# Performance work log

Hardware: AMD Instinct MI355X
Metric: run time of the kernel (lower is better)

The kernel has to match this reference:

```python
import jax, jax.numpy as jnp
import numpy as np

N_NODES = 50000
N_EDGES = 800000
FEAT = 64
HID = 128
N_TYPES = 4
N_REL = 3
N_LAYERS = 2
LN_EPS = 1e-5


def setup_inputs() -> dict:
    key = jax.random.key(0)
    ks = jax.random.split(key, 20)
    inp = {
        "z": jax.random.randint(ks[0], (N_NODES,), 0, 100, dtype=jnp.int32),
        "node_type": jax.random.randint(ks[1], (N_NODES,), 0, N_TYPES, dtype=jnp.int32),
        "edge_index": jax.random.randint(ks[2], (2, N_EDGES), 0, N_NODES, dtype=jnp.int32),
        "edge_type": jax.random.randint(ks[3], (N_EDGES,), 0, N_REL, dtype=jnp.int32),
        # learned parameters
        "z_embed": jax.random.normal(ks[4], (100, FEAT), jnp.float32),
        "enc_w1": jax.random.normal(ks[5], (N_TYPES, FEAT, HID), jnp.float32) * 0.05,
        "enc_b1": jnp.zeros((N_TYPES, HID), jnp.float32),
        "enc_w2": jax.random.normal(ks[6], (N_TYPES, HID, HID), jnp.float32) * 0.05,
        "enc_b2": jnp.zeros((N_TYPES, HID), jnp.float32),
        "lin_w": jax.random.normal(ks[7], (N_LAYERS, HID, HID), jnp.float32) * 0.05,
        "lin_b": jnp.zeros((N_LAYERS, HID), jnp.float32),
        "rel_w": jax.random.normal(ks[8], (N_LAYERS, N_REL, HID, HID), jnp.float32) * 0.05,
        "ln_g": jnp.ones((N_LAYERS, HID), jnp.float32),
        "ln_b": jnp.zeros((N_LAYERS, HID), jnp.float32),
        "reg_w": jax.random.normal(ks[9], (HID, 1), jnp.float32) * 0.05,
        "reg_b": jnp.zeros((1,), jnp.float32),
    }
    return inp


def _layer_norm(x, g, b):
    mu = jnp.mean(x, axis=-1, keepdims=True)
    var = jnp.mean((x - mu) ** 2, axis=-1, keepdims=True)
    return (x - mu) * jax.lax.rsqrt(var + LN_EPS) * g + b


def reference(z, node_type, edge_index, edge_type, z_embed, enc_w1, enc_b1,
              enc_w2, enc_b2, lin_w, lin_b, rel_w, ln_g, ln_b, reg_w, reg_b):
    n = z.shape[0]
    # FeatureBuilder (site_ads=None path): atomic-number embedding lookup
    raw = z_embed[z]  # [N, FEAT]
    # TypeSpecificEncoder: run all 4 type MLPs, select per node by node_type
    h = jax.nn.relu(jnp.einsum('nd,tdh->nth', raw, enc_w1) + enc_b1)  # [N,T,H]
    enc_all = jnp.einsum('nth,tho->nto', h, enc_w2) + enc_b2           # [N,T,H]
    x = jnp.take_along_axis(enc_all, node_type[:, None, None].astype(jnp.int32), axis=1)[:, 0, :]

    src, dst = edge_index[0], edge_index[1]
    deg = jax.ops.segment_sum(jnp.ones((edge_type.shape[0],), x.dtype), dst, num_segments=n)
    deg = jnp.clip(deg, 1.0, None)[:, None]  # [N,1]

    for l in range(N_LAYERS):
        out = jnp.zeros_like(x)
        x_src = x[src]  # [E, H] gathered source features
        for r in range(N_REL):
            mask = (edge_type == r).astype(x.dtype)[:, None]
            msg = (x_src * mask) @ rel_w[l, r]  # [E, H]
            out = out + jax.ops.segment_sum(msg, dst, num_segments=n)
        out = out / deg
        x = _layer_norm(x @ lin_w[l] + lin_b[l] + out, ln_g[l], ln_b[l])

    pooled = jnp.mean(x, axis=0)  # mean pooling, mask = all ones
    return pooled @ reg_w + reg_b  # [1]
```

## Files before the change

### kernel.cpp

```cpp
#include <hip/hip_runtime.h>

#define N_NODES 50000
#define N_EDGES 800000
#define FEAT 64
#define HID 128
#define N_TYPES 4
#define N_REL 3
#define N_LAYERS 2
#define LN_EPS 1e-5f
#define NROWS 50016
#define NG32 1563
#define CAP 64
#define NBKT 196
#define CAP1 4608
#define EPB 4096
#define BINCAP 56
#define NCOMBO 400
#define WT_STRIDE 136

typedef __attribute__((ext_vector_type(8))) short bf16x8;
typedef __attribute__((ext_vector_type(16))) float f32x16;

static __device__ inline unsigned short f2bf(float f) {
    unsigned int u = __float_as_uint(f);
    return (unsigned short)((u + 0x7fffu + ((u >> 16) & 1u)) >> 16);
}
static __device__ inline unsigned int packbf2(float lo, float hi) {
    return (unsigned int)f2bf(lo) | ((unsigned int)f2bf(hi) << 16);
}

__global__ __launch_bounds__(256) void combo_kernel(const int* __restrict__ z,
                                                    const int* __restrict__ nt,
                                                    unsigned short* __restrict__ combo) {
    int i = blockIdx.x * 256 + threadIdx.x;
    if (i < N_NODES) combo[i] = (unsigned short)(z[i] * 4 + nt[i]);
}

__global__ __launch_bounds__(256) void bin1_kernel(const int* __restrict__ src,
                                                   const int* __restrict__ dst,
                                                   const int* __restrict__ et,
                                                   int* __restrict__ bcnt,
                                                   int* __restrict__ bucket) {
    __shared__ int lbin[NBKT * BINCAP];
    __shared__ int lcnt[NBKT];
    __shared__ int lbase[NBKT];
    for (int i = threadIdx.x; i < NBKT; i += 256) lcnt[i] = 0;
    __syncthreads();
    int base = blockIdx.x * EPB;
#pragma unroll
    for (int i = 0; i < EPB / 256; ++i) {
        int e = base + i * 256 + threadIdx.x;
        if (e < N_EDGES) {
            int d = dst[e];
            int b = d >> 8;
            int v = src[e] | (et[e] << 16) | ((d & 255) << 18);
            int pos = atomicAdd(&lcnt[b], 1);
            if (pos < BINCAP) lbin[b * BINCAP + pos] = v;
        }
    }
    __syncthreads();
    if (threadIdx.x < NBKT) {
        int c = min(lcnt[threadIdx.x], BINCAP);
        lcnt[threadIdx.x] = c;
        lbase[threadIdx.x] = atomicAdd(&bcnt[threadIdx.x], c);
    }
    __syncthreads();
    int wv = threadIdx.x >> 6, ln = threadIdx.x & 63;
    for (int b = wv; b < NBKT; b += 4) {
        int c = lcnt[b];
        if (ln < c) {
            int gp = lbase[b] + ln;
            if (gp < CAP1) bucket[b * CAP1 + gp] = lbin[b * BINCAP + ln];
        }
    }
}

__global__ __launch_bounds__(256) void build2_kernel(const int* __restrict__ bcnt,
                                                     const int* __restrict__ bucket,
                                                     const unsigned short* __restrict__ combo,
                                                     int* __restrict__ cnt,
                                                     int* __restrict__ payload) {
    __shared__ int lcnt[256];
    lcnt[threadIdx.x] = 0;
    __syncthreads();
    int b = blockIdx.x;
    int n0 = b << 8;
    int cb = min(bcnt[b], CAP1);
    const int* bk = bucket + b * CAP1;
    for (int i = threadIdx.x; i < cb; i += 256) {
        int v = bk[i];
        int dl = (v >> 18) & 255;
        int sc = v & 0xffff;
        int pos = atomicAdd(&lcnt[dl], 1);
        if (pos < CAP)
            payload[((n0 + dl) << 6) + pos] = (v & 0x3FFFF) | ((int)combo[sc] << 18);
    }
    __syncthreads();
    int node = n0 + threadIdx.x;
    if (node < N_NODES) cnt[node] = min(lcnt[threadIdx.x], CAP);
}

__global__ __launch_bounds__(128) void enc_table_kernel(const float* __restrict__ z_embed,
                                                        const float* __restrict__ w1,
                                                        const float* __restrict__ b1,
                                                        const float* __restrict__ w2,
                                                        const float* __restrict__ b2,
                                                        unsigned short* __restrict__ xt) {
    int zi = blockIdx.x >> 2;
    int t = blockIdx.x & 3;
    int j = threadIdx.x;
    __shared__ float h[HID];
    float acc = b1[t * HID + j];
#pragma unroll 8
    for (int k = 0; k < FEAT; ++k)
        acc = fmaf(z_embed[zi * FEAT + k], w1[((size_t)t * FEAT + k) * HID + j], acc);
    h[j] = fmaxf(acc, 0.0f);
    __syncthreads();
    float acc2 = b2[t * HID + j];
#pragma unroll 8
    for (int k = 0; k < HID; ++k)
        acc2 = fmaf(h[k], w2[(size_t)t * HID * HID + k * HID + j], acc2);
    xt[blockIdx.x * HID + j] = f2bf(acc2);
}

__global__ __launch_bounds__(128) void rel_table_kernel(const unsigned short* __restrict__ xt,
                                                        const float* __restrict__ rel_w,
                                                        const float* __restrict__ lin_w,
                                                        const float* __restrict__ lin_b,
                                                        unsigned short* __restrict__ ytab,
                                                        float* __restrict__ lintab) {
    int c = blockIdx.x;
    int j = threadIdx.x;
    __shared__ float xrow[HID];
    xrow[j] = __uint_as_float((unsigned int)xt[c * HID + j] << 16);
    __syncthreads();
#pragma unroll 1
    for (int r = 0; r < N_REL; ++r) {
        float acc = 0.f;
        const float* W = rel_w + (size_t)r * HID * HID;
#pragma unroll 8
        for (int k = 0; k < HID; ++k) acc = fmaf(xrow[k], W[k * HID + j], acc);
        ytab[(size_t)(r * NCOMBO + c) * HID + j] = f2bf(acc);
    }
    float acc = lin_b[j];
#pragma unroll 8
    for (int k = 0; k < HID; ++k) acc = fmaf(xrow[k], lin_w[k * HID + j], acc);
    lintab[c * HID + j] = acc;
}

__global__ __launch_bounds__(256) void prep_weights_kernel(const float* __restrict__ rel_w,
                                                           const float* __restrict__ lin_w,
                                                           unsigned short* __restrict__ wbuf) {
    int idx = blockIdx.x * 256 + threadIdx.x;
    if (idx >= 2 * 4 * HID * HID) return;
    int k = idx & 127;
    int col = (idx >> 7) & 127;
    int lm = idx >> 14;
    int l = lm >> 2, mat = lm & 3;
    float w = (mat < 3) ? rel_w[(((size_t)l * 3 + mat) * HID + k) * HID + col]
                        : lin_w[((size_t)l * HID + k) * HID + col];
    wbuf[(size_t)lm * HID * WT_STRIDE + col * WT_STRIDE + k] = f2bf(w);
}

__global__ __launch_bounds__(256) void gather_ln1_kernel(
    const int* __restrict__ cnt, const int* __restrict__ payload,
    const uint4* __restrict__ ytab4, const float* __restrict__ lintab,
    const unsigned short* __restrict__ combo, const float* __restrict__ lng,
    const float* __restrict__ lnb, uint4* __restrict__ xb4) {
    int tid = blockIdx.x * 256 + threadIdx.x;
    int node = tid >> 4;
    int l16 = tid & 15;
    int cn = cnt[node];
    float inv = 1.0f / (float)max(cn, 1);
    const int* pl = payload + (node << 6);
    float a[8] = {};
    int e = 0;
    for (; e + 2 <= cn; e += 2) {
        int pA = pl[e], pB = pl[e + 1];
        uint4 vA = ytab4[((((pA >> 16) & 3) * NCOMBO + (pA >> 18)) << 4) + l16];
        uint4 vB = ytab4[((((pB >> 16) & 3) * NCOMBO + (pB >> 18)) << 4) + l16];
        a[0] += __uint_as_float(vA.x << 16) + __uint_as_float(vB.x << 16);
        a[1] += __uint_as_float(vA.x & 0xffff0000u) + __uint_as_float(vB.x & 0xffff0000u);
        a[2] += __uint_as_float(vA.y << 16) + __uint_as_float(vB.y << 16);
        a[3] += __uint_as_float(vA.y & 0xffff0000u) + __uint_as_float(vB.y & 0xffff0000u);
        a[4] += __uint_as_float(vA.z << 16) + __uint_as_float(vB.z << 16);
        a[5] += __uint_as_float(vA.z & 0xffff0000u) + __uint_as_float(vB.z & 0xffff0000u);
        a[6] += __uint_as_float(vA.w << 16) + __uint_as_float(vB.w << 16);
        a[7] += __uint_as_float(vA.w & 0xffff0000u) + __uint_as_float(vB.w & 0xffff0000u);
    }
    if (e < cn) {
        int p = pl[e];
        uint4 v = ytab4[((((p >> 16) & 3) * NCOMBO + (p >> 18)) << 4) + l16];
        a[0] += __uint_as_float(v.x << 16);
        a[1] += __uint_as_float(v.x & 0xffff0000u);
        a[2] += __uint_as_float(v.y << 16);
        a[3] += __uint_as_float(v.y & 0xffff0000u);
        a[4] += __uint_as_float(v.z << 16);
        a[5] += __uint_as_float(v.z & 0xffff0000u);
        a[6] += __uint_as_float(v.w << 16);
        a[7] += __uint_as_float(v.w & 0xffff0000u);
    }
    const float* lrow = lintab + (int)combo[node] * HID + l16 * 8;
    float v[8], s = 0.f, q = 0.f;
#pragma unroll
    for (int j = 0; j < 8; ++j) {
        v[j] = fmaf(a[j], inv, lrow[j]);
        s += v[j];
        q += v[j] * v[j];
    }
#pragma unroll
    for (int mk = 1; mk < 16; mk <<= 1) {
        s += __shfl_xor(s, mk);
        q += __shfl_xor(q, mk);
    }
    float mu = s * (1.0f / HID);
    float rstd = rsqrtf(q * (1.0f / HID) - mu * mu + LN_EPS);
    const float* g8 = lng + l16 * 8;
    const float* b8 = lnb + l16 * 8;
    uint4 w;
    w.x = packbf2((v[0] - mu) * rstd * g8[0] + b8[0], (v[1] - mu) * rstd * g8[1] + b8[1]);
    w.y = packbf2((v[2] - mu) * rstd * g8[2] + b8[2], (v[3] - mu) * rstd * g8[3] + b8[3]);
    w.z = packbf2((v[4] - mu) * rstd * g8[4] + b8[4], (v[5] - mu) * rstd * g8[5] + b8[5]);
    w.w = packbf2((v[6] - mu) * rstd * g8[6] + b8[6], (v[7] - mu) * rstd * g8[7] + b8[7]);
    xb4[(node << 4) + l16] = w;
}

__global__ __launch_bounds__(256) void gather3_kernel(const int* __restrict__ cnt,
                                                      const int* __restrict__ payload,
                                                      const uint4* __restrict__ xb4,
                                                      uint4* __restrict__ s0,
                                                      uint4* __restrict__ s1,
                                                      uint4* __restrict__ s2) {
    int tid = blockIdx.x * 256 + threadIdx.x;
    int node = tid >> 4;
    int l16 = tid & 15;
    int cn = cnt[node];
    float inv = 1.0f / (float)max(cn, 1);
    const int* pl = payload + (node << 6);
    float a0[8] = {}, a1[8] = {}, a2[8] = {};

    int e = 0;
    for (; e + 2 <= cn; e += 2) {
        int pA = pl[e];
        int pB = pl[e + 1];
        uint4 vA = xb4[(pA & 0xffff) * 16 + l16];
        uint4 vB = xb4[(pB & 0xffff) * 16 + l16];
        float fA[8] = {__uint_as_float(vA.x << 16), __uint_as_float(vA.x & 0xffff0000u),
                       __uint_as_float(vA.y << 16), __uint_as_float(vA.y & 0xffff0000u),
                       __uint_as_float(vA.z << 16), __uint_as_float(vA.z & 0xffff0000u),
                       __uint_as_float(vA.w << 16), __uint_as_float(vA.w & 0xffff0000u)};
        float fB[8] = {__uint_as_float(vB.x << 16), __uint_as_float(vB.x & 0xffff0000u),
                       __uint_as_float(vB.y << 16), __uint_as_float(vB.y & 0xffff0000u),
                       __uint_as_float(vB.z << 16), __uint_as_float(vB.z & 0xffff0000u),
                       __uint_as_float(vB.w << 16), __uint_as_float(vB.w & 0xffff0000u)};
        int rA = (pA >> 16) & 3, rB = (pB >> 16) & 3;
#pragma unroll
        for (int j = 0; j < 8; ++j) {
            if (rA == 0) a0[j] += fA[j];
            else if (rA == 1) a1[j] += fA[j];
            else a2[j] += fA[j];
            if (rB == 0) a0[j] += fB[j];
            else if (rB == 1) a1[j] += fB[j];
            else a2[j] += fB[j];
        }
    }
    if (e < cn) {
        int p = pl[e];
        uint4 v = xb4[(p & 0xffff) * 16 + l16];
        float f[8] = {__uint_as_float(v.x << 16), __uint_as_float(v.x & 0xffff0000u),
                      __uint_as_float(v.y << 16), __uint_as_float(v.y & 0xffff0000u),
                      __uint_as_float(v.z << 16), __uint_as_float(v.z & 0xffff0000u),
                      __uint_as_float(v.w << 16), __uint_as_float(v.w & 0xffff0000u)};
        int r = (p >> 16) & 3;
#pragma unroll
        for (int j = 0; j < 8; ++j) {
            if (r == 0) a0[j] += f[j];
            else if (r == 1) a1[j] += f[j];
            else a2[j] += f[j];
        }
    }
    int o = node * 16 + l16;
    uint4 w;
    w.x = packbf2(a0[0] * inv, a0[1] * inv); w.y = packbf2(a0[2] * inv, a0[3] * inv);
    w.z = packbf2(a0[4] * inv, a0[5] * inv); w.w = packbf2(a0[6] * inv, a0[7] * inv);
    s0[o] = w;
    w.x = packbf2(a1[0] * inv, a1[1] * inv); w.y = packbf2(a1[2] * inv, a1[3] * inv);
    w.z = packbf2(a1[4] * inv, a1[5] * inv); w.w = packbf2(a1[6] * inv, a1[7] * inv);
    s1[o] = w;
    w.x = packbf2(a2[0] * inv, a2[1] * inv); w.y = packbf2(a2[2] * inv, a2[3] * inv);
    w.z = packbf2(a2[4] * inv, a2[5] * inv); w.w = packbf2(a2[6] * inv, a2[7] * inv);
    s2[o] = w;
}

__global__ __launch_bounds__(512) void fused_layer_kernel(
    const unsigned short* __restrict__ s0, const unsigned short* __restrict__ s1,
    const unsigned short* __restrict__ s2, unsigned short* __restrict__ xb,
    const uint4* __restrict__ wbuf, const float* __restrict__ lb,
    const float* __restrict__ lng, const float* __restrict__ lnb,
    float* __restrict__ pooled, int do_pool) {
    __shared__ __align__(16) unsigned short Wt[4 * HID * WT_STRIDE];
    __shared__ float csh[3 * HID];
    __shared__ float pooled_sh[HID];

    if (threadIdx.x < HID) {
        pooled_sh[threadIdx.x] = 0.0f;
        csh[threadIdx.x] = lb[threadIdx.x];
        csh[HID + threadIdx.x] = lng[threadIdx.x];
        csh[2 * HID + threadIdx.x] = lnb[threadIdx.x];
    }
    uint4* wt4 = (uint4*)Wt;
#pragma unroll
    for (int i = 0; i < 17; ++i)
        wt4[i * 512 + threadIdx.x] = wbuf[i * 512 + threadIdx.x];
    __syncthreads();

    int wave = threadIdx.x >> 6;
    int lane = threadIdx.x & 63;
    int n32 = lane & 31;
    int hf = lane >> 5;

    float pacc[4] = {0.f, 0.f, 0.f, 0.f};

    for (int g = wave * gridDim.x + blockIdx.x; g < NG32; g += gridDim.x * 8) {
        int node0 = g * 32;
        f32x16 acc[4];
#pragma unroll
        for (int ct = 0; ct < 4; ++ct)
#pragma unroll
            for (int i = 0; i < 16; ++i) acc[ct][i] = 0.0f;

#pragma unroll 1
        for (int mat = 0; mat < 4; ++mat) {
            const unsigned short* asrc = (mat == 0) ? s0 : (mat == 1) ? s1
                                       : (mat == 2) ? s2 : xb;
            const unsigned short* arow = asrc + (size_t)(node0 + n32) * HID + hf * 8;
            const unsigned short* wm = Wt + mat * (HID * WT_STRIDE) + n32 * WT_STRIDE + hf * 8;
#pragma unroll 2
            for (int t = 0; t < 8; ++t) {
                bf16x8 a = *(const bf16x8*)(arow + t * 16);
#pragma unroll
                for (int ct = 0; ct < 4; ++ct) {
                    bf16x8 b = *(const bf16x8*)(wm + ct * 32 * WT_STRIDE + t * 16);
                    acc[ct] = __builtin_amdgcn_mfma_f32_32x32x16_bf16(a, b, acc[ct], 0, 0, 0);
                }
            }
        }
#pragma unroll
        for (int reg = 0; reg < 16; ++reg) {
            int row = node0 + (reg & 3) + 8 * (reg >> 2) + 4 * hf;
            float v[4];
            float s = 0.f, q = 0.f;
#pragma unroll
            for (int ct = 0; ct < 4; ++ct) {
                v[ct] = acc[ct][reg] + csh[ct * 32 + n32];
                s += v[ct];
                q += v[ct] * v[ct];
            }
#pragma unroll
            for (int mk = 1; mk < 32; mk <<= 1) {
                s += __shfl_xor(s, mk);
                q += __shfl_xor(q, mk);
            }
            float mu = s * (1.0f / HID);
            float rstd = rsqrtf(q * (1.0f / HID) - mu * mu + LN_EPS);
#pragma unroll
            for (int ct = 0; ct < 4; ++ct) {
                int col = ct * 32 + n32;
                float outv = (v[ct] - mu) * rstd * csh[HID + col] + csh[2 * HID + col];
                if (do_pool) {
                    if (row < N_NODES) pacc[ct] += outv;
                } else {
                    xb[(size_t)row * HID + col] = f2bf(outv);
                }
            }
        }
    }

    if (do_pool) {
#pragma unroll
        for (int ct = 0; ct < 4; ++ct) {
            float t = pacc[ct] + __shfl_xor(pacc[ct], 32);
            if (hf == 0) atomicAdd(&pooled_sh[ct * 32 + n32], t);
        }
        __syncthreads();
        if (threadIdx.x < HID) atomicAdd(&pooled[threadIdx.x], pooled_sh[threadIdx.x]);
    }
}

__global__ void final_kernel(const float* __restrict__ pooled, const float* __restrict__ reg_w,
                             const float* __restrict__ reg_b, float* __restrict__ out) {
    int lane = threadIdx.x;
    float s = pooled[lane] * reg_w[lane] + pooled[64 + lane] * reg_w[64 + lane];
#pragma unroll
    for (int o = 32; o; o >>= 1) s += __shfl_down(s, o);
    if (lane == 0) out[0] = s * (1.0f / N_NODES) + reg_b[0];
}

extern "C" void kernel_launch(void* const* d_in, const int* in_sizes, int n_in,
                              void* d_out, int out_size, void* d_ws, size_t ws_size,
                              hipStream_t stream) {
    const int* z = (const int*)d_in[0];
    const int* nt = (const int*)d_in[1];
    const int* ei = (const int*)d_in[2];
    const int* et = (const int*)d_in[3];
    const float* z_embed = (const float*)d_in[4];
    const float* enc_w1 = (const float*)d_in[5];
    const float* enc_b1 = (const float*)d_in[6];
    const float* enc_w2 = (const float*)d_in[7];
    const float* enc_b2 = (const float*)d_in[8];
    const float* lin_w = (const float*)d_in[9];
    const float* lin_b = (const float*)d_in[10];
    const float* rel_w = (const float*)d_in[11];
    const float* ln_g = (const float*)d_in[12];
    const float* ln_b = (const float*)d_in[13];
    const float* reg_w = (const float*)d_in[14];
    const float* reg_b = (const float*)d_in[15];
    float* out = (float*)d_out;

    const size_t NHb = (size_t)NROWS * HID;
    char* p = (char*)d_ws;
    unsigned short* xb = (unsigned short*)p;    p += NHb * 2;
    unsigned short* s0 = (unsigned short*)p;    p += NHb * 2;
    unsigned short* s1 = (unsigned short*)p;    p += NHb * 2;
    unsigned short* s2 = (unsigned short*)p;    p += NHb * 2;
    unsigned short* wbuf = (unsigned short*)p;  p += (size_t)8 * HID * WT_STRIDE * 2;
    unsigned short* xt = (unsigned short*)p;    p += NCOMBO * HID * 2;
    unsigned short* ytab = (unsigned short*)p;  p += (size_t)N_REL * NCOMBO * HID * 2;
    float* lintab = (float*)p;                  p += NCOMBO * HID * 4;
    unsigned short* combo = (unsigned short*)p; p += N_NODES * 2;
    float* pooled = (float*)p;                  p += HID * 4;
    int* cnt = (int*)p;                         p += N_NODES * 4;
    int* bcnt = (int*)p;                        p += NBKT * 4;
    int* bucket = (int*)p;                      p += (size_t)NBKT * CAP1 * 4;
    int* payload = (int*)p;                     p += (size_t)N_NODES * CAP * 4;

    const int* src = ei;
    const int* dst = ei + N_EDGES;

    hipMemsetAsync(bcnt, 0, NBKT * sizeof(int), stream);
    hipMemsetAsync(pooled, 0, HID * sizeof(float), stream);
    combo_kernel<<<NBKT, 256, 0, stream>>>(z, nt, combo);
    bin1_kernel<<<NBKT, 256, 0, stream>>>(src, dst, et, bcnt, bucket);
    build2_kernel<<<NBKT, 256, 0, stream>>>(bcnt, bucket, combo, cnt, payload);

    enc_table_kernel<<<NCOMBO, 128, 0, stream>>>(z_embed, enc_w1, enc_b1, enc_w2, enc_b2, xt);
    rel_table_kernel<<<NCOMBO, 128, 0, stream>>>(xt, rel_w, lin_w, lin_b, ytab, lintab);
    prep_weights_kernel<<<512, 256, 0, stream>>>(rel_w, lin_w, wbuf);

    gather_ln1_kernel<<<3125, 256, 0, stream>>>(cnt, payload, (const uint4*)ytab, lintab,
                                                combo, ln_g, ln_b, (uint4*)xb);
    gather3_kernel<<<3125, 256, 0, stream>>>(cnt, payload, (const uint4*)xb,
                                             (uint4*)s0, (uint4*)s1, (uint4*)s2);
    const uint4* wl = (const uint4*)(wbuf + (size_t)1 * 4 * HID * WT_STRIDE);
    fused_layer_kernel<<<256, 512, 0, stream>>>(
        s0, s1, s2, xb, wl, lin_b + HID, ln_g + HID, ln_b + HID, pooled, 1);

    final_kernel<<<1, 64, 0, stream>>>(pooled, reg_w, reg_b, out);
}
```

Baseline: 254.1 us.

## Sort edge payload by relation and fuse encoder/relation table kernels

```diff
diff --git a/kernel.cpp b/kernel.cpp
--- a/kernel.cpp
+++ b/kernel.cpp
@@ -78,10 +78,10 @@
 __global__ __launch_bounds__(256) void build2_kernel(const int* __restrict__ bcnt,
                                                      const int* __restrict__ bucket,
                                                      const unsigned short* __restrict__ combo,
-                                                     int* __restrict__ cnt,
+                                                     int* __restrict__ cnt3,
                                                      int* __restrict__ payload) {
-    __shared__ int lcnt[256];
-    lcnt[threadIdx.x] = 0;
+    __shared__ int lcnt[256 * 3];
+    for (int i = threadIdx.x; i < 768; i += 256) lcnt[i] = 0;
     __syncthreads();
     int b = blockIdx.x;
     int n0 = b << 8;
@@ -89,27 +89,47 @@
     const int* bk = bucket + b * CAP1;
     for (int i = threadIdx.x; i < cb; i += 256) {
         int v = bk[i];
+        atomicAdd(&lcnt[((v >> 18) & 255) * 3 + ((v >> 16) & 3)], 1);
+    }
+    __syncthreads();
+    int t = threadIdx.x;
+    int c0 = min(lcnt[t * 3 + 0], CAP);
+    int c1 = min(lcnt[t * 3 + 1], CAP - c0);
+    int c2 = min(lcnt[t * 3 + 2], CAP - c0 - c1);
+    __syncthreads();
+    lcnt[t * 3 + 0] = 0;
+    lcnt[t * 3 + 1] = c0;
+    lcnt[t * 3 + 2] = c0 + c1;
+    int node = n0 + t;
+    if (node < N_NODES) cnt3[node] = c0 | (c1 << 8) | (c2 << 16);
+    __syncthreads();
+    for (int i = threadIdx.x; i < cb; i += 256) {
+        int v = bk[i];
         int dl = (v >> 18) & 255;
+        int r = (v >> 16) & 3;
         int sc = v & 0xffff;
-        int pos = atomicAdd(&lcnt[dl], 1);
+        int pos = atomicAdd(&lcnt[dl * 3 + r], 1);
         if (pos < CAP)
-            payload[((n0 + dl) << 6) + pos] = (v & 0x3FFFF) | ((int)combo[sc] << 18);
-    }
-    __syncthreads();
-    int node = n0 + threadIdx.x;
-    if (node < N_NODES) cnt[node] = min(lcnt[threadIdx.x], CAP);
-}
-
-__global__ __launch_bounds__(128) void enc_table_kernel(const float* __restrict__ z_embed,
-                                                        const float* __restrict__ w1,
-                                                        const float* __restrict__ b1,
-                                                        const float* __restrict__ w2,
-                                                        const float* __restrict__ b2,
-                                                        unsigned short* __restrict__ xt) {
-    int zi = blockIdx.x >> 2;
-    int t = blockIdx.x & 3;
+            payload[((n0 + dl) << 6) + pos] = sc | ((int)combo[sc] << 18);
+    }
+}
+
+__global__ __launch_bounds__(128) void table_kernel(const float* __restrict__ z_embed,
+                                                    const float* __restrict__ w1,
+                                                    const float* __restrict__ b1,
+                                                    const float* __restrict__ w2,
+                                                    const float* __restrict__ b2,
+                                                    const float* __restrict__ rel_w,
+                                                    const float* __restrict__ lin_w,
+                                                    const float* __restrict__ lin_b,
+                                                    unsigned short* __restrict__ ytab,
+                                                    float* __restrict__ lintab) {
+    int c = blockIdx.x;
+    int zi = c >> 2;
+    int t = c & 3;
     int j = threadIdx.x;
     __shared__ float h[HID];
+    __shared__ float xrow[HID];
     float acc = b1[t * HID + j];
 #pragma unroll 8
     for (int k = 0; k < FEAT; ++k)
@@ -120,85 +140,79 @@
 #pragma unroll 8
     for (int k = 0; k < HID; ++k)
         acc2 = fmaf(h[k], w2[(size_t)t * HID * HID + k * HID + j], acc2);
-    xt[blockIdx.x * HID + j] = f2bf(acc2);
-}
-
-__global__ __launch_bounds__(128) void rel_table_kernel(const unsigned short* __restrict__ xt,
-                                                        const float* __restrict__ rel_w,
-                                                        const float* __restrict__ lin_w,
-                                                        const float* __restrict__ lin_b,
-                                                        unsigned short* __restrict__ ytab,
-                                                        float* __restrict__ lintab) {
-    int c = blockIdx.x;
-    int j = threadIdx.x;
-    __shared__ float xrow[HID];
-    xrow[j] = __uint_as_float((unsigned int)xt[c * HID + j] << 16);
+    xrow[j] = acc2;
     __syncthreads();
 #pragma unroll 1
     for (int r = 0; r < N_REL; ++r) {
-        float acc = 0.f;
+        float a = 0.f;
         const float* W = rel_w + (size_t)r * HID * HID;
 #pragma unroll 8
-        for (int k = 0; k < HID; ++k) acc = fmaf(xrow[k], W[k * HID + j], acc);
-        ytab[(size_t)(r * NCOMBO + c) * HID + j] = f2bf(acc);
-    }
-    float acc = lin_b[j];
+        for (int k = 0; k < HID; ++k) a = fmaf(xrow[k], W[k * HID + j], a);
+        ytab[(size_t)(r * NCOMBO + c) * HID + j] = f2bf(a);
+    }
+    float a = lin_b[j];
 #pragma unroll 8
-    for (int k = 0; k < HID; ++k) acc = fmaf(xrow[k], lin_w[k * HID + j], acc);
-    lintab[c * HID + j] = acc;
+    for (int k = 0; k < HID; ++k) a = fmaf(xrow[k], lin_w[k * HID + j], a);
+    lintab[c * HID + j] = a;
 }
 
 __global__ __launch_bounds__(256) void prep_weights_kernel(const float* __restrict__ rel_w,
                                                            const float* __restrict__ lin_w,
                                                            unsigned short* __restrict__ wbuf) {
     int idx = blockIdx.x * 256 + threadIdx.x;
-    if (idx >= 2 * 4 * HID * HID) return;
+    if (idx >= 4 * HID * HID) return;
     int k = idx & 127;
     int col = (idx >> 7) & 127;
-    int lm = idx >> 14;
-    int l = lm >> 2, mat = lm & 3;
-    float w = (mat < 3) ? rel_w[(((size_t)l * 3 + mat) * HID + k) * HID + col]
-                        : lin_w[((size_t)l * HID + k) * HID + col];
-    wbuf[(size_t)lm * HID * WT_STRIDE + col * WT_STRIDE + k] = f2bf(w);
+    int mat = idx >> 14;
+    float w = (mat < 3) ? rel_w[(((size_t)(3 + mat)) * HID + k) * HID + col]
+                        : lin_w[((size_t)(HID + k)) * HID + col];
+    wbuf[(size_t)mat * HID * WT_STRIDE + col * WT_STRIDE + k] = f2bf(w);
 }
 
 __global__ __launch_bounds__(256) void gather_ln1_kernel(
-    const int* __restrict__ cnt, const int* __restrict__ payload,
+    const int* __restrict__ cnt3, const int* __restrict__ payload,
     const uint4* __restrict__ ytab4, const float* __restrict__ lintab,
     const unsigned short* __restrict__ combo, const float* __restrict__ lng,
     const float* __restrict__ lnb, uint4* __restrict__ xb4) {
     int tid = blockIdx.x * 256 + threadIdx.x;
     int node = tid >> 4;
     int l16 = tid & 15;
-    int cn = cnt[node];
-    float inv = 1.0f / (float)max(cn, 1);
+    int c3 = cnt3[node];
+    int c0 = c3 & 255, c1 = (c3 >> 8) & 255, c2 = (c3 >> 16) & 255;
+    int tot = c0 + c1 + c2;
+    float inv = 1.0f / (float)max(tot, 1);
     const int* pl = payload + (node << 6);
     float a[8] = {};
     int e = 0;
-    for (; e + 2 <= cn; e += 2) {
-        int pA = pl[e], pB = pl[e + 1];
-        uint4 vA = ytab4[((((pA >> 16) & 3) * NCOMBO + (pA >> 18)) << 4) + l16];
-        uint4 vB = ytab4[((((pB >> 16) & 3) * NCOMBO + (pB >> 18)) << 4) + l16];
-        a[0] += __uint_as_float(vA.x << 16) + __uint_as_float(vB.x << 16);
-        a[1] += __uint_as_float(vA.x & 0xffff0000u) + __uint_as_float(vB.x & 0xffff0000u);
-        a[2] += __uint_as_float(vA.y << 16) + __uint_as_float(vB.y << 16);
-        a[3] += __uint_as_float(vA.y & 0xffff0000u) + __uint_as_float(vB.y & 0xffff0000u);
-        a[4] += __uint_as_float(vA.z << 16) + __uint_as_float(vB.z << 16);
-        a[5] += __uint_as_float(vA.z & 0xffff0000u) + __uint_as_float(vB.z & 0xffff0000u);
-        a[6] += __uint_as_float(vA.w << 16) + __uint_as_float(vB.w << 16);
-        a[7] += __uint_as_float(vA.w & 0xffff0000u) + __uint_as_float(vB.w & 0xffff0000u);
-    }
-    if (e < cn) {
-        int p = pl[e];
-        uint4 v = ytab4[((((p >> 16) & 3) * NCOMBO + (p >> 18)) << 4) + l16];
-        a[0] += __uint_as_float(v.x << 16);
-        a[1] += __uint_as_float(v.x & 0xffff0000u);
-        a[2] += __uint_as_float(v.y << 16);
-        a[3] += __uint_as_float(v.y & 0xffff0000u);
-        a[4] += __uint_as_float(v.z << 16);
-        a[5] += __uint_as_float(v.z & 0xffff0000u);
-        a[6] += __uint_as_float(v.w << 16);
-        a[7] += __uint_as_float(v.w & 0xffff0000u);
+#pragma unroll 1
+    for (int r = 0; r < 3; ++r) {
+        int e1 = (r == 0) ? c0 : (r == 1) ? c0 + c1 : tot;
+        int base = (r * NCOMBO) << 4;
+        for (; e + 2 <= e1; e += 2) {
+            int pA = pl[e], pB = pl[e + 1];
+            uint4 vA = ytab4[base + ((pA >> 18) << 4) + l16];
+            uint4 vB = ytab4[base + ((pB >> 18) << 4) + l16];
+            a[0] += __uint_as_float(vA.x << 16) + __uint_as_float(vB.x << 16);
+            a[1] += __uint_as_float(vA.x & 0xffff0000u) + __uint_as_float(vB.x & 0xffff0000u);
+            a[2] += __uint_as_float(vA.y << 16) + __uint_as_float(vB.y << 16);
+            a[3] += __uint_as_float(vA.y & 0xffff0000u) + __uint_as_float(vB.y & 0xffff0000u);
+            a[4] += __uint_as_float(vA.z << 16) + __uint_as_float(vB.z << 16);
+            a[5] += __uint_as_float(vA.z & 0xffff0000u) + __uint_as_float(vB.z & 0xffff0000u);
+            a[6] += __uint_as_float(vA.w << 16) + __uint_as_float(vB.w << 16);
+            a[7] += __uint_as_float(vA.w & 0xffff0000u) + __uint_as_float(vB.w & 0xffff0000u);
+        }
+        if (e < e1) {
+            int p = pl[e]; ++e;
+            uint4 v = ytab4[base + ((p >> 18) << 4) + l16];
+            a[0] += __uint_as_float(v.x << 16);
+            a[1] += __uint_as_float(v.x & 0xffff0000u);
+            a[2] += __uint_as_float(v.y << 16);
+            a[3] += __uint_as_float(v.y & 0xffff0000u);
+            a[4] += __uint_as_float(v.z << 16);
+            a[5] += __uint_as_float(v.z & 0xffff0000u);
+            a[6] += __uint_as_float(v.w << 16);
+            a[7] += __uint_as_float(v.w & 0xffff0000u);
+        }
     }
     const float* lrow = lintab + (int)combo[node] * HID + l16 * 8;
     float v[8], s = 0.f, q = 0.f;
@@ -225,7 +239,7 @@
     xb4[(node << 4) + l16] = w;
 }
 
-__global__ __launch_bounds__(256) void gather3_kernel(const int* __restrict__ cnt,
+__global__ __launch_bounds__(256) void gather3_kernel(const int* __restrict__ cnt3,
                                                       const int* __restrict__ payload,
                                                       const uint4* __restrict__ xb4,
                                                       uint4* __restrict__ s0,
@@ -234,70 +248,59 @@
     int tid = blockIdx.x * 256 + threadIdx.x;
     int node = tid >> 4;
     int l16 = tid & 15;
-    int cn = cnt[node];
-    float inv = 1.0f / (float)max(cn, 1);
+    int c3 = cnt3[node];
+    int c0 = c3 & 255, c1 = (c3 >> 8) & 255, c2 = (c3 >> 16) & 255;
+    int tot = c0 + c1 + c2;
+    float inv = 1.0f / (float)max(tot, 1);
     const int* pl = payload + (node << 6);
-    float a0[8] = {}, a1[8] = {}, a2[8] = {};
-
+    int o = node * 16 + l16;
     int e = 0;
-    for (; e + 2 <= cn; e += 2) {
-        int pA = pl[e];
-        int pB = pl[e + 1];
-        uint4 vA = xb4[(pA & 0xffff) * 16 + l16];
-        uint4 vB = xb4[(pB & 0xffff) * 16 + l16];
-        float fA[8] = {__uint_as_float(vA.x << 16), __uint_as_float(vA.x & 0xffff0000u),
-                       __uint_as_float(vA.y << 16), __uint_as_float(vA.y & 0xffff0000u),
-                       __uint_as_float(vA.z << 16), __uint_as_float(vA.z & 0xffff0000u),
-                       __uint_as_float(vA.w << 16), __uint_as_float(vA.w & 0xffff0000u)};
-        float fB[8] = {__uint_as_float(vB.x << 16), __uint_as_float(vB.x & 0xffff0000u),
-                       __uint_as_float(vB.y << 16), __uint_as_float(vB.y & 0xffff0000u),
-                       __uint_as_float(vB.z << 16), __uint_as_float(vB.z & 0xffff0000u),
-                       __uint_as_float(vB.w << 16), __uint_as_float(vB.w & 0xffff0000u)};
-        int rA = (pA >> 16) & 3, rB = (pB >> 16) & 3;
-#pragma unroll
-        for (int j = 0; j < 8; ++j) {
-            if (rA == 0) a0[j] += fA[j];
-            else if (rA == 1) a1[j] += fA[j];
-            else a2[j] += fA[j];
-            if (rB == 0) a0[j] += fB[j];
-            else if (rB == 1) a1[j] += fB[j];
-            else a2[j] += fB[j];
-        }
-    }
-    if (e < cn) {
-        int p = pl[e];
-        uint4 v = xb4[(p & 0xffff) * 16 + l16];
-        float f[8] = {__uint_as_float(v.x << 16), __uint_as_float(v.x & 0xffff0000u),
-                      __uint_as_float(v.y << 16), __uint_as_float(v.y & 0xffff0000u),
-                      __uint_as_float(v.z << 16), __uint_as_float(v.z & 0xffff0000u),
-                      __uint_as_float(v.w << 16), __uint_as_float(v.w & 0xffff0000u)};
-        int r = (p >> 16) & 3;
-#pragma unroll
-        for (int j = 0; j < 8; ++j) {
-            if (r == 0) a0[j] += f[j];
-            else if (r == 1) a1[j] += f[j];
-            else a2[j] += f[j];
-        }
-    }
-    int o = node * 16 + l16;
-    uint4 w;
-    w.x = packbf2(a0[0] * inv, a0[1] * inv); w.y = packbf2(a0[2] * inv, a0[3] * inv);
-    w.z = packbf2(a0[4] * inv, a0[5] * inv); w.w = packbf2(a0[6] * inv, a0[7] * inv);
-    s0[o] = w;
-    w.x = packbf2(a1[0] * inv, a1[1] * inv); w.y = packbf2(a1[2] * inv, a1[3] * inv);
-    w.z = packbf2(a1[4] * inv, a1[5] * inv); w.w = packbf2(a1[6] * inv, a1[7] * inv);
-    s1[o] = w;
-    w.x = packbf2(a2[0] * inv, a2[1] * inv); w.y = packbf2(a2[2] * inv, a2[3] * inv);
-    w.z = packbf2(a2[4] * inv, a2[5] * inv); w.w = packbf2(a2[6] * inv, a2[7] * inv);
-    s2[o] = w;
+#pragma unroll 1
+    for (int r = 0; r < 3; ++r) {
+        int e1 = (r == 0) ? c0 : (r == 1) ? c0 + c1 : tot;
+        float a[8] = {};
+        for (; e + 2 <= e1; e += 2) {
+            int pA = pl[e], pB = pl[e + 1];
+            uint4 vA = xb4[((pA & 0xffff) << 4) + l16];
+            uint4 vB = xb4[((pB & 0xffff) << 4) + l16];
+            a[0] += __uint_as_float(vA.x << 16) + __uint_as_float(vB.x << 16);
+            a[1] += __uint_as_float(vA.x & 0xffff0000u) + __uint_as_float(vB.x & 0xffff0000u);
+            a[2] += __uint_as_float(vA.y << 16) + __uint_as_float(vB.y << 16);
+            a[3] += __uint_as_float(vA.y & 0xffff0000u) + __uint_as_float(vB.y & 0xffff0000u);
+            a[4] += __uint_as_float(vA.z << 16) + __uint_as_float(vB.z << 16);
+            a[5] += __uint_as_float(vA.z & 0xffff0000u) + __uint_as_float(vB.z & 0xffff0000u);
+            a[6] += __uint_as_float(vA.w << 16) + __uint_as_float(vB.w << 16);
+            a[7] += __uint_as_float(vA.w & 0xffff0000u) + __uint_as_float(vB.w & 0xffff0000u);
+        }
+        if (e < e1) {
+            int p = pl[e]; ++e;
+            uint4 v = xb4[((p & 0xffff) << 4) + l16];
+            a[0] += __uint_as_float(v.x << 16);
+            a[1] += __uint_as_float(v.x & 0xffff0000u);
+            a[2] += __uint_as_float(v.y << 16);
+            a[3] += __uint_as_float(v.y & 0xffff0000u);
+            a[4] += __uint_as_float(v.z << 16);
+            a[5] += __uint_as_float(v.z & 0xffff0000u);
+            a[6] += __uint_as_float(v.w << 16);
+            a[7] += __uint_as_float(v.w & 0xffff0000u);
+        }
+        uint4 w;
+        w.x = packbf2(a[0] * inv, a[1] * inv);
+        w.y = packbf2(a[2] * inv, a[3] * inv);
+        w.z = packbf2(a[4] * inv, a[5] * inv);
+        w.w = packbf2(a[6] * inv, a[7] * inv);
+        if (r == 0) s0[o] = w;
+        else if (r == 1) s1[o] = w;
+        else s2[o] = w;
+    }
 }
 
 __global__ __launch_bounds__(512) void fused_layer_kernel(
     const unsigned short* __restrict__ s0, const unsigned short* __restrict__ s1,
-    const unsigned short* __restrict__ s2, unsigned short* __restrict__ xb,
+    const unsigned short* __restrict__ s2, const unsigned short* __restrict__ xb,
     const uint4* __restrict__ wbuf, const float* __restrict__ lb,
     const float* __restrict__ lng, const float* __restrict__ lnb,
-    float* __restrict__ pooled, int do_pool) {
+    float* __restrict__ pooled) {
     __shared__ __align__(16) unsigned short Wt[4 * HID * WT_STRIDE];
     __shared__ float csh[3 * HID];
     __shared__ float pooled_sh[HID];
@@ -363,28 +366,23 @@
             }
             float mu = s * (1.0f / HID);
             float rstd = rsqrtf(q * (1.0f / HID) - mu * mu + LN_EPS);
-#pragma unroll
-            for (int ct = 0; ct < 4; ++ct) {
-                int col = ct * 32 + n32;
-                float outv = (v[ct] - mu) * rstd * csh[HID + col] + csh[2 * HID + col];
-                if (do_pool) {
-                    if (row < N_NODES) pacc[ct] += outv;
-                } else {
-                    xb[(size_t)row * HID + col] = f2bf(outv);
+            if (row < N_NODES) {
+#pragma unroll
+                for (int ct = 0; ct < 4; ++ct) {
+                    int col = ct * 32 + n32;
+                    pacc[ct] += (v[ct] - mu) * rstd * csh[HID + col] + csh[2 * HID + col];
                 }
             }
         }
     }
 
-    if (do_pool) {
-#pragma unroll
-        for (int ct = 0; ct < 4; ++ct) {
-            float t = pacc[ct] + __shfl_xor(pacc[ct], 32);
-            if (hf == 0) atomicAdd(&pooled_sh[ct * 32 + n32], t);
-        }
-        __syncthreads();
-        if (threadIdx.x < HID) atomicAdd(&pooled[threadIdx.x], pooled_sh[threadIdx.x]);
-    }
+#pragma unroll
+    for (int ct = 0; ct < 4; ++ct) {
+        float t = pacc[ct] + __shfl_xor(pacc[ct], 32);
+        if (hf == 0) atomicAdd(&pooled_sh[ct * 32 + n32], t);
+    }
+    __syncthreads();
+    if (threadIdx.x < HID) atomicAdd(&pooled[threadIdx.x], pooled_sh[threadIdx.x]);
 }
 
 __global__ void final_kernel(const float* __restrict__ pooled, const float* __restrict__ reg_w,
@@ -423,13 +421,12 @@
     unsigned short* s0 = (unsigned short*)p;    p += NHb * 2;
     unsigned short* s1 = (unsigned short*)p;    p += NHb * 2;
     unsigned short* s2 = (unsigned short*)p;    p += NHb * 2;
-    unsigned short* wbuf = (unsigned short*)p;  p += (size_t)8 * HID * WT_STRIDE * 2;
-    unsigned short* xt = (unsigned short*)p;    p += NCOMBO * HID * 2;
+    unsigned short* wbuf = (unsigned short*)p;  p += (size_t)4 * HID * WT_STRIDE * 2;
     unsigned short* ytab = (unsigned short*)p;  p += (size_t)N_REL * NCOMBO * HID * 2;
     float* lintab = (float*)p;                  p += NCOMBO * HID * 4;
     unsigned short* combo = (unsigned short*)p; p += N_NODES * 2;
     float* pooled = (float*)p;                  p += HID * 4;
-    int* cnt = (int*)p;                         p += N_NODES * 4;
+    int* cnt3 = (int*)p;                        p += N_NODES * 4;
     int* bcnt = (int*)p;                        p += NBKT * 4;
     int* bucket = (int*)p;                      p += (size_t)NBKT * CAP1 * 4;
     int* payload = (int*)p;                     p += (size_t)N_NODES * CAP * 4;
@@ -441,19 +438,18 @@
     hipMemsetAsync(pooled, 0, HID * sizeof(float), stream);
     combo_kernel<<<NBKT, 256, 0, stream>>>(z, nt, combo);
     bin1_kernel<<<NBKT, 256, 0, stream>>>(src, dst, et, bcnt, bucket);
-    build2_kernel<<<NBKT, 256, 0, stream>>>(bcnt, bucket, combo, cnt, payload);
-
-    enc_table_kernel<<<NCOMBO, 128, 0, stream>>>(z_embed, enc_w1, enc_b1, enc_w2, enc_b2, xt);
-    rel_table_kernel<<<NCOMBO, 128, 0, stream>>>(xt, rel_w, lin_w, lin_b, ytab, lintab);
-    prep_weights_kernel<<<512, 256, 0, stream>>>(rel_w, lin_w, wbuf);
-
-    gather_ln1_kernel<<<3125, 256, 0, stream>>>(cnt, payload, (const uint4*)ytab, lintab,
+    build2_kernel<<<NBKT, 256, 0, stream>>>(bcnt, bucket, combo, cnt3, payload);
+
+    table_kernel<<<NCOMBO, 128, 0, stream>>>(z_embed, enc_w1, enc_b1, enc_w2, enc_b2,
+                                             rel_w, lin_w, lin_b, ytab, lintab);
+    prep_weights_kernel<<<256, 256, 0, stream>>>(rel_w, lin_w, wbuf);
+
+    gather_ln1_kernel<<<3125, 256, 0, stream>>>(cnt3, payload, (const uint4*)ytab, lintab,
                                                 combo, ln_g, ln_b, (uint4*)xb);
-    gather3_kernel<<<3125, 256, 0, stream>>>(cnt, payload, (const uint4*)xb,
+    gather3_kernel<<<3125, 256, 0, stream>>>(cnt3, payload, (const uint4*)xb,
                                              (uint4*)s0, (uint4*)s1, (uint4*)s2);
-    const uint4* wl = (const uint4*)(wbuf + (size_t)1 * 4 * HID * WT_STRIDE);
     fused_layer_kernel<<<256, 512, 0, stream>>>(
-        s0, s1, s2, xb, wl, lin_b + HID, ln_g + HID, ln_b + HID, pooled, 1);
+        s0, s1, s2, xb, (const uint4*)wbuf, lin_b + HID, ln_g + HID, ln_b + HID, pooled);
 
     final_kernel<<<1, 64, 0, stream>>>(pooled, reg_w, reg_b, out);
 }
```

New measurement: 247.5 us. -2.6%, faster.
